# Optimization experiments

Measured on AMD Instinct MI355X. Metric: run time of the kernel, lower is better.

Reference implementation:

```python
import jax, jax.numpy as jnp
import numpy as np

B, M, N, D, K, H = 128, 64, 128, 10, 4, 64
DT = 1.0 / 128.0      # eqn_config.dt
ALPHA = 1.0           # net_config.alpha
STRIKE = 0.4          # basket-call strike (option.payoff)


def setup_inputs() -> dict:
    key = jax.random.key(0)
    ks = jax.random.split(key, 8)
    t = jax.random.uniform(ks[0], (B, M, N, 1), dtype=jnp.float32)
    x = jax.random.uniform(ks[1], (B, M, N, D), dtype=jnp.float32)
    dw = jax.random.normal(ks[2], (B, M, N - 1, D), dtype=jnp.float32) * (DT ** 0.5)
    u_hat = jax.random.uniform(ks[3], (B, M, N, K), dtype=jnp.float32)
    zin = 1 + D + K
    W1 = jax.random.normal(ks[4], (zin, H), dtype=jnp.float32) / np.float32(np.sqrt(zin))
    W2 = jax.random.normal(ks[5], (H, H), dtype=jnp.float32) / np.float32(np.sqrt(H))
    W3 = jax.random.normal(ks[6], (H, 1), dtype=jnp.float32) / np.float32(np.sqrt(H))
    b1 = jnp.zeros((H,), jnp.float32)
    b2 = jnp.zeros((H,), jnp.float32)
    b3 = jnp.zeros((1,), jnp.float32)
    return {"t": t, "x": x, "dw": dw, "u_hat": u_hat,
            "W1": W1, "b1": b1, "W2": W2, "b2": b2, "W3": W3, "b3": b3}


def _mlp(t, x, u, W1, b1, W2, b2, W3, b3):
    # net_forward: (t, x, u_hat) -> value f, shape (B, M, N, 1)
    z = jnp.concatenate([t, x, u], axis=-1)
    h = jnp.tanh(z @ W1 + b1)
    h = jnp.tanh(h @ W2 + b2)
    return h @ W3 + b3


def reference(t, x, dw, u_hat, W1, b1, W2, b2, W3, b3):
    # f and df/dx (tape.gradient(f, x) == vjp with ones cotangent)
    f, vjp_fn = jax.vjp(lambda xx: _mlp(t, xx, u_hat, W1, b1, W2, b2, W3, b3), x)
    grad = vjp_fn(jnp.ones_like(f))[0]                 # (B, M, N, D)

    f_now = f[:, :, :-1, :]                            # (B, M, N-1, 1)
    f_pls = f[:, :, 1:, :]
    grad_now = grad[:, :, :-1, :]
    x_now = x[:, :, :-1, :]
    r = u_hat[:, :, :-1, 0:1]                          # GBM rate param
    sigma = u_hat[:, :, :-1, 1:2]                      # GBM vol param

    # drift_bsde = r*y ; diffusion_bsde = sum(sigma*x*grad*dw, -1)
    drift = r * f_now
    z = jnp.sum(sigma * x_now * grad_now * dw, axis=-1, keepdims=True)
    V_hat = f_now - drift * DT + z                     # (B, M, N-1, 1)
    diff = f_pls - V_hat

    # suffix sums over the time axis: tele[n] = sum_{k>=n} diff[k]
    tele = jnp.flip(jnp.cumsum(jnp.flip(diff, axis=2), axis=2), axis=2)  # (B, M, N-1, 1)

    # payoff: European basket call on terminal state, shape (B, M, 1)
    payoff = jax.nn.relu(jnp.mean(x[:, :, -1, :], axis=-1, keepdims=True) - STRIKE)
    f_T = f_pls[:, :, -1, :]                           # (B, M, 1)

    resid = tele + (payoff - f_T)[:, :, None, :]       # (B, M, N-1, 1)
    # loss_interior = sum_n mean_{B,M}(resid_n^2)
    loss_interior = jnp.sum(jnp.mean(jnp.square(resid), axis=(0, 1, 3)))
    loss_tml = jnp.mean(jnp.square(f_T - payoff))
    loss = ALPHA * loss_tml + loss_interior
    return (loss, loss_interior, loss_tml)
```

## Files before the change

### kernel.cpp

```cpp
#include <hip/hip_runtime.h>

#define B_ 128
#define M_ 64
#define N_ 128
#define D_ 10
#define K_ 4
#define H_ 64
#define DT_ (1.0f/128.0f)
#define STRIKE_ 0.4f

__device__ __forceinline__ float fast_tanh(float x) {
    x = fminf(30.f, fmaxf(-30.f, x));
    float e = __builtin_amdgcn_exp2f(x * -2.885390081777927f);
    return (1.f - e) * __builtin_amdgcn_rcpf(1.f + e);
}

extern "C" __global__ void solver_setup(const float* __restrict__ W1,
                                        float* __restrict__ W1T,
                                        float* gI, float* gT) {
    int h = threadIdx.x;
    if (h == 0) { *gI = 0.f; *gT = 0.f; }
    #pragma unroll
    for (int d = 0; d < 16; ++d)
        W1T[h * 16 + d] = (d < D_) ? W1[(1 + d) * H_ + h] : 0.f;
}

extern "C" __global__ void __launch_bounds__(256, 2)
solver_main(const float* __restrict__ tt, const float* __restrict__ xx,
            const float* __restrict__ dw, const float* __restrict__ uu,
            const float* __restrict__ W1, const float* __restrict__ b1,
            const float* __restrict__ W2, const float* __restrict__ b2,
            const float* __restrict__ W3, const float* __restrict__ b3,
            const float* __restrict__ W1T,
            float* __restrict__ gI, float* __restrict__ gT)
{
    __shared__ _Float16 A1[H_ * 256];
    __shared__ float payLDS[2];
    __shared__ float wtotLDS[2];
    __shared__ float wsum[2][2];

    const int tid  = threadIdx.x;
    const int path = tid >> 7;
    const int n    = tid & 127;
    const int bm   = blockIdx.x * 2 + path;
    const int p    = bm * N_ + n;

    float tval = tt[p];
    float xr[D_];
    {
        const float2* v = reinterpret_cast<const float2*>(xx + (size_t)p * D_);
        #pragma unroll
        for (int i = 0; i < 5; ++i) { float2 w = v[i]; xr[2*i] = w.x; xr[2*i+1] = w.y; }
    }
    float4 uv = *reinterpret_cast<const float4*>(uu + (size_t)p * K_);
    float dwr[D_];
    if (n < N_ - 1) {
        const float2* v = reinterpret_cast<const float2*>(dw + ((size_t)bm * (N_-1) + n) * D_);
        #pragma unroll
        for (int i = 0; i < 5; ++i) { float2 w = v[i]; dwr[2*i] = w.x; dwr[2*i+1] = w.y; }
    } else {
        #pragma unroll
        for (int i = 0; i < D_; ++i) dwr[i] = 0.f;
    }
    float r_ = uv.x, sigma = uv.y;
    float a[D_];
    #pragma unroll
    for (int d = 0; d < D_; ++d) a[d] = sigma * xr[d] * dwr[d];

    if (n == N_ - 1) {
        float s = 0.f;
        #pragma unroll
        for (int d = 0; d < D_; ++d) s += xr[d];
        payLDS[path] = fmaxf(s * (1.f / D_) - STRIKE_, 0.f);
    }

    float acc[H_];
    #pragma unroll
    for (int h = 0; h < H_; ++h) acc[h] = b1[h];
    #pragma unroll
    for (int h = 0; h < H_; ++h) acc[h] = fmaf(tval, W1[h], acc[h]);
    #pragma unroll
    for (int i = 0; i < D_; ++i) {
        const float* w = W1 + (1 + i) * H_;
        float zi = xr[i];
        #pragma unroll
        for (int h = 0; h < H_; ++h) acc[h] = fmaf(zi, w[h], acc[h]);
    }
    {
        float ur[K_] = {uv.x, uv.y, uv.z, uv.w};
        #pragma unroll
        for (int i = 0; i < K_; ++i) {
            const float* w = W1 + (1 + D_ + i) * H_;
            #pragma unroll
            for (int h = 0; h < H_; ++h) acc[h] = fmaf(ur[i], w[h], acc[h]);
        }
    }

    #pragma unroll
    for (int h = 0; h < H_; ++h) A1[h * 256 + tid] = (_Float16)fast_tanh(acc[h]);

    #pragma unroll
    for (int h = 0; h < H_; ++h) acc[h] = b2[h];
    #pragma unroll 1
    for (int i = 0; i < H_; ++i) {
        float h1i = (float)A1[i * 256 + tid];
        const float* w = W2 + i * H_;
        #pragma unroll
        for (int h = 0; h < H_; ++h) acc[h] = fmaf(h1i, w[h], acc[h]);
    }

    float fp[8];
    #pragma unroll
    for (int j = 0; j < 8; ++j) fp[j] = 0.f;
    #pragma unroll
    for (int h = 0; h < H_; ++h) {
        float h2 = fast_tanh(acc[h]);
        float w3 = W3[h];
        fp[h & 7] = fmaf(w3, h2, fp[h & 7]);
        acc[h] = w3 * (1.f - h2 * h2);
    }
    float f = ((fp[0]+fp[4]) + (fp[1]+fp[5])) + ((fp[2]+fp[6]) + (fp[3]+fp[7]));
    f += b3[0];

    float zt[4]; zt[0] = zt[1] = zt[2] = zt[3] = 0.f;
    #pragma unroll 1
    for (int i = 0; i < H_; ++i) {
        const float* w = W2 + i * H_;
        float pp[8];
        #pragma unroll
        for (int j = 0; j < 8; ++j) pp[j] = 0.f;
        #pragma unroll
        for (int h = 0; h < H_; ++h) pp[h & 7] = fmaf(w[h], acc[h], pp[h & 7]);
        float gpre = ((pp[0]+pp[4]) + (pp[1]+pp[5])) + ((pp[2]+pp[6]) + (pp[3]+pp[7]));
        float h1i = (float)A1[i * 256 + tid];
        float g1 = gpre * (1.f - h1i * h1i);
        const float* wt = W1T + i * 16;
        float q = 0.f;
        #pragma unroll
        for (int d = 0; d < D_; ++d) q = fmaf(a[d], wt[d], q);
        zt[i & 3] = fmaf(g1, q, zt[i & 3]);
    }
    float zterm = (zt[0] + zt[2]) + (zt[1] + zt[3]);

    float cn = (n < N_ - 1) ? fmaf(r_ * f, DT_, -zterm) : 0.f;

    float S = cn;
    #pragma unroll
    for (int off = 1; off < 64; off <<= 1) {
        float o = __shfl_down(S, off);
        S += (((n & 63) + off) < 64) ? o : 0.f;
    }
    if (n == 64) wtotLDS[path] = S;
    __syncthreads();
    if (n < 64) S += wtotLDS[path];
    float pay = payLDS[path];

    float resid = (n < N_ - 1) ? (pay - f + S) : 0.f;
    float v = resid * resid;
    #pragma unroll
    for (int off = 32; off; off >>= 1) v += __shfl_down(v, off);
    if ((n & 63) == 0) wsum[path][n >> 6] = v;
    __syncthreads();
    if (n == 0) atomicAdd(gI, wsum[path][0] + wsum[path][1]);
    if (n == N_ - 1) { float d0 = f - pay; atomicAdd(gT, d0 * d0); }
}

extern "C" __global__ void solver_fin(const float* gI, const float* gT, float* out) {
    float li = *gI * (1.f / (B_ * M_));
    float lt = *gT * (1.f / (B_ * M_));
    out[0] = 1.0f * lt + li;
    out[1] = li;
    out[2] = lt;
}

extern "C" void kernel_launch(void* const* d_in, const int* in_sizes, int n_in,
                              void* d_out, int out_size, void* d_ws, size_t ws_size,
                              hipStream_t stream) {
    const float* tt = (const float*)d_in[0];
    const float* xx = (const float*)d_in[1];
    const float* dw = (const float*)d_in[2];
    const float* uu = (const float*)d_in[3];
    const float* W1 = (const float*)d_in[4];
    const float* b1 = (const float*)d_in[5];
    const float* W2 = (const float*)d_in[6];
    const float* b2 = (const float*)d_in[7];
    const float* W3 = (const float*)d_in[8];
    const float* b3 = (const float*)d_in[9];
    float* out = (float*)d_out;
    float* ws  = (float*)d_ws;
    float* gI  = ws;
    float* gT  = ws + 1;
    float* W1T = ws + 8;

    hipLaunchKernelGGL(solver_setup, dim3(1), dim3(64), 0, stream, W1, W1T, gI, gT);
    hipLaunchKernelGGL(solver_main, dim3(B_ * M_ / 2), dim3(256), 0, stream,
                       tt, xx, dw, uu, W1, b1, W2, b2, W3, b3, W1T, gI, gT);
    hipLaunchKernelGGL(solver_fin, dim3(1), dim3(1), 0, stream, gI, gT, out);
}
```

Before: 501.6 us.

## Compute diffusion term by forward-mode tangent propagation fused into layer-2 loop

The separate backward pass through W2 is replaced by a forward-mode directional derivative. The tangent v_i = (1-h1_i^2)·(W1x^T a)_i is pushed through W2 in the same loop that computes the layer-2 pre-activations. The result is then contracted with w3·(1-h2^2) in the output loop. W2 is traversed once instead of twice, and the per-row 8-way reductions of the old backward loop are gone. The cost is a second 64-entry register array per thread, which raises VGPR pressure and could cut occupancy or cause spills.

New measurement: 467.9 us. 6.7% less time.

```diff
diff --git a/kernel.cpp b/kernel.cpp
--- a/kernel.cpp
+++ b/kernel.cpp
@@ -68,10 +68,10 @@
     for (int d = 0; d < D_; ++d) a[d] = sigma * xr[d] * dwr[d];
 
     if (n == N_ - 1) {
-        float s = 0.f;
+        float s0 = 0.f;
         #pragma unroll
-        for (int d = 0; d < D_; ++d) s += xr[d];
-        payLDS[path] = fmaxf(s * (1.f / D_) - STRIKE_, 0.f);
+        for (int d = 0; d < D_; ++d) s0 += xr[d];
+        payLDS[path] = fmaxf(s0 * (1.f / D_) - STRIKE_, 0.f);
     }
 
     float acc[H_];
@@ -99,48 +99,37 @@
     #pragma unroll
     for (int h = 0; h < H_; ++h) A1[h * 256 + tid] = (_Float16)fast_tanh(acc[h]);
 
+    float s[H_];
     #pragma unroll
-    for (int h = 0; h < H_; ++h) acc[h] = b2[h];
+    for (int h = 0; h < H_; ++h) { acc[h] = b2[h]; s[h] = 0.f; }
     #pragma unroll 1
     for (int i = 0; i < H_; ++i) {
         float h1i = (float)A1[i * 256 + tid];
-        const float* w = W2 + i * H_;
+        const float* w  = W2 + i * H_;
+        const float* wt = W1T + i * 16;
+        float q = 0.f;
         #pragma unroll
-        for (int h = 0; h < H_; ++h) acc[h] = fmaf(h1i, w[h], acc[h]);
+        for (int d = 0; d < D_; ++d) q = fmaf(a[d], wt[d], q);
+        float v = (1.f - h1i * h1i) * q;
+        #pragma unroll
+        for (int h = 0; h < H_; ++h) {
+            acc[h] = fmaf(h1i, w[h], acc[h]);
+            s[h]   = fmaf(v,   w[h], s[h]);
+        }
     }
 
-    float fp[8];
-    #pragma unroll
-    for (int j = 0; j < 8; ++j) fp[j] = 0.f;
+    float fp[4] = {0.f, 0.f, 0.f, 0.f};
+    float zp[4] = {0.f, 0.f, 0.f, 0.f};
     #pragma unroll
     for (int h = 0; h < H_; ++h) {
         float h2 = fast_tanh(acc[h]);
         float w3 = W3[h];
-        fp[h & 7] = fmaf(w3, h2, fp[h & 7]);
-        acc[h] = w3 * (1.f - h2 * h2);
+        fp[h & 3] = fmaf(w3, h2, fp[h & 3]);
+        float g2h = w3 * (1.f - h2 * h2);
+        zp[h & 3] = fmaf(g2h, s[h], zp[h & 3]);
     }
-    float f = ((fp[0]+fp[4]) + (fp[1]+fp[5])) + ((fp[2]+fp[6]) + (fp[3]+fp[7]));
-    f += b3[0];
-
-    float zt[4]; zt[0] = zt[1] = zt[2] = zt[3] = 0.f;
-    #pragma unroll 1
-    for (int i = 0; i < H_; ++i) {
-        const float* w = W2 + i * H_;
-        float pp[8];
-        #pragma unroll
-        for (int j = 0; j < 8; ++j) pp[j] = 0.f;
-        #pragma unroll
-        for (int h = 0; h < H_; ++h) pp[h & 7] = fmaf(w[h], acc[h], pp[h & 7]);
-        float gpre = ((pp[0]+pp[4]) + (pp[1]+pp[5])) + ((pp[2]+pp[6]) + (pp[3]+pp[7]));
-        float h1i = (float)A1[i * 256 + tid];
-        float g1 = gpre * (1.f - h1i * h1i);
-        const float* wt = W1T + i * 16;
-        float q = 0.f;
-        #pragma unroll
-        for (int d = 0; d < D_; ++d) q = fmaf(a[d], wt[d], q);
-        zt[i & 3] = fmaf(g1, q, zt[i & 3]);
-    }
-    float zterm = (zt[0] + zt[2]) + (zt[1] + zt[3]);
+    float f = (fp[0] + fp[2]) + (fp[1] + fp[3]) + b3[0];
+    float zterm = (zp[0] + zp[2]) + (zp[1] + zp[3]);
 
     float cn = (n < N_ - 1) ? fmaf(r_ * f, DT_, -zterm) : 0.f;
 
@@ -156,10 +145,10 @@
     float pay = payLDS[path];
 
     float resid = (n < N_ - 1) ? (pay - f + S) : 0.f;
-    float v = resid * resid;
+    float v2 = resid * resid;
     #pragma unroll
-    for (int off = 32; off; off >>= 1) v += __shfl_down(v, off);
-    if ((n & 63) == 0) wsum[path][n >> 6] = v;
+    for (int off = 32; off; off >>= 1) v2 += __shfl_down(v2, off);
+    if ((n & 63) == 0) wsum[path][n >> 6] = v2;
     __syncthreads();
     if (n == 0) atomicAdd(gI, wsum[path][0] + wsum[path][1]);
     if (n == N_ - 1) { float d0 = f - pay; atomicAdd(gT, d0 * d0); }
```
